# Kernel optimization log

Measured on AMD Instinct MI355X. Metric: run time of the kernel, lower is better.

## Reference

```python
import jax, jax.numpy as jnp
import numpy as np

B, S, HID = 4, 128, 4096
D, HQ, HK = 128, 32, 8
PAGES, PSIZE, NPP = 64, 256, 16  # page pool, page size, pages per sequence
THETA = 10000.0
EPS = 1e-6
SCALE = 1.0 / float(np.sqrt(D))


def setup_inputs() -> dict:
    key = jax.random.key(0)
    ks = jax.random.split(key, 10)
    x = jax.random.normal(ks[0], (B, S, HID), jnp.float32)
    Wq = jax.random.normal(ks[1], (HQ * D, HID), jnp.float32) * 0.02
    Wk = jax.random.normal(ks[2], (HK * D, HID), jnp.float32) * 0.02
    Wv = jax.random.normal(ks[3], (HK * D, HID), jnp.float32) * 0.02
    Wo = jax.random.normal(ks[4], (HID, HQ * D), jnp.float32) * 0.02
    q_norm_w = jax.random.uniform(ks[5], (D,), jnp.float32)
    k_norm_w = jax.random.uniform(ks[6], (D,), jnp.float32)
    k_cache = jax.random.normal(ks[7], (PAGES, PSIZE, HK, D), jnp.float32)
    v_cache = jax.random.normal(ks[8], (PAGES, PSIZE, HK, D), jnp.float32)
    block_table = jnp.arange(B * NPP, dtype=jnp.int32).reshape(B, NPP)
    cache_seqlens = jax.random.randint(ks[9], (B,), 0, 3800).astype(jnp.int32)
    return dict(x=x, Wq=Wq, Wk=Wk, Wv=Wv, Wo=Wo, q_norm_w=q_norm_w,
                k_norm_w=k_norm_w, k_cache=k_cache, v_cache=v_cache,
                block_table=block_table, cache_seqlens=cache_seqlens)


def _rmsnorm(t, w):
    # per-head RMSNorm over head_dim (constant_bias = 0)
    var = jnp.mean(t * t, axis=-1, keepdims=True)
    return t * jax.lax.rsqrt(var + EPS) * w


def _rope(t, pos):
    # NeoX-style half-rotation. t: [B,S,H,D], pos: [B,S]
    inv_freq = 1.0 / (THETA ** (jnp.arange(0, D, 2, dtype=jnp.float32) / D))  # [D/2]
    freqs = pos[..., None].astype(jnp.float32) * inv_freq                     # [B,S,D/2]
    cos = jnp.cos(freqs)[:, :, None, :]
    sin = jnp.sin(freqs)[:, :, None, :]
    t1, t2 = t[..., : D // 2], t[..., D // 2:]
    return jnp.concatenate([t1 * cos - t2 * sin, t2 * cos + t1 * sin], axis=-1)


def reference(x, Wq, Wk, Wv, Wo, q_norm_w, k_norm_w, k_cache, v_cache,
              block_table, cache_seqlens):
    bsz, seqlen, _ = x.shape
    # QKV projections
    q = jnp.einsum('bsd,ed->bse', x, Wq).reshape(bsz, seqlen, HQ, D)
    k = jnp.einsum('bsd,ed->bse', x, Wk).reshape(bsz, seqlen, HK, D)
    v = jnp.einsum('bsd,ed->bse', x, Wv).reshape(bsz, seqlen, HK, D)
    # QK-norm then RoPE (fused norm+rope path of the module)
    q = _rmsnorm(q, q_norm_w)
    k = _rmsnorm(k, k_norm_w)
    pos = cache_seqlens[:, None] + jnp.arange(seqlen)[None, :]  # [B,S]
    q = _rope(q, pos)
    k = _rope(k, pos)
    # Gather paged KV cache: [B, NPP*PSIZE, HK, D]
    L = NPP * PSIZE
    kc = k_cache[block_table].reshape(bsz, L, HK, D)
    vc = v_cache[block_table].reshape(bsz, L, HK, D)
    # Append new tokens (flash_attn_with_kvcache writes k,v into the cache)
    k_all = jnp.concatenate([kc, k], axis=1)  # [B, L+S, HK, D]
    v_all = jnp.concatenate([vc, v], axis=1)
    # Valid mask: cache slots < cache_seqlens; all new keys valid (causal=False, full window)
    valid_c = jnp.arange(L)[None, :] < cache_seqlens[:, None]          # [B, L]
    valid = jnp.concatenate(
        [valid_c, jnp.ones((bsz, seqlen), dtype=bool)], axis=1)        # [B, L+S]
    rep = HQ // HK
    k_all = jnp.repeat(k_all, rep, axis=2)
    v_all = jnp.repeat(v_all, rep, axis=2)
    scores = jnp.einsum('bqhd,bkhd->bhqk', q, k_all) * SCALE
    scores = jnp.where(valid[:, None, None, :], scores, -1e30)
    probs = jax.nn.softmax(scores, axis=-1)
    o = jnp.einsum('bhqk,bkhd->bqhd', probs, v_all)
    o = o.reshape(bsz, seqlen, HQ * D)
    return jnp.einsum('bse,de->bsd', o, Wo)
```

## Files before the change

### kernel.cpp

```cpp
#include <hip/hip_runtime.h>

typedef unsigned short u16;
typedef float f4v __attribute__((ext_vector_type(4)));
typedef short s8v __attribute__((ext_vector_type(8)));
typedef int   i4v __attribute__((ext_vector_type(4)));

#define SCALE_ 0.08838834764831845f
#define LOG2E_ 1.44269504088896340f

__device__ __forceinline__ u16 f2b(float f) {
    union { float f; unsigned u; } c; c.f = f;
    unsigned u = c.u + 0x7fffu + ((c.u >> 16) & 1u);
    return (u16)(u >> 16);
}

typedef const __attribute__((address_space(1))) unsigned int gu32;
typedef __attribute__((address_space(3))) unsigned int lu32;
__device__ __forceinline__ void glds16(const void* g, void* l) {
    __builtin_amdgcn_global_load_lds((gu32*)g, (lu32*)l, 16, 0, 0);
}

__device__ __forceinline__ int rho(int kv) {
    return (kv & 0x20) | ((kv & 0x04) << 2) | ((kv & 0x18) >> 1) | (kv & 3);
}

template <int RB>
__global__ __launch_bounds__(256) void wcvt_k(const float* __restrict__ src,
                                              u16* __restrict__ dst, int K) {
    const int kt = blockIdx.x, nt = blockIdx.y;
    u16* out = dst + ((size_t)nt * gridDim.x + kt) * (RB * 64);
#pragma unroll
    for (int i = 0; i < RB / 32; i++) {
        int c = threadIdx.x + i * 256;
        int r = c >> 3, c16 = c & 7, cc = c16 ^ (r & 7);
        const float* p = src + (size_t)(nt * RB + r) * K + kt * 64 + cc * 8;
        float4 f0 = *(const float4*)p, f1 = *(const float4*)(p + 4);
        s8v v;
        v[0] = (short)f2b(f0.x); v[1] = (short)f2b(f0.y);
        v[2] = (short)f2b(f0.z); v[3] = (short)f2b(f0.w);
        v[4] = (short)f2b(f1.x); v[5] = (short)f2b(f1.y);
        v[6] = (short)f2b(f1.z); v[7] = (short)f2b(f1.w);
        *(s8v*)(out + r * 64 + c16 * 8) = v;
    }
}

__global__ __launch_bounds__(256) void fgemm2(const u16* __restrict__ Ag,
                                              const u16* __restrict__ Bg,
                                              float* __restrict__ Cp,
                                              int M, int N, int K, int Ksl,
                                              int NY, int NZ) {
    __shared__ __align__(16) u16 As[2][4096];
    __shared__ __align__(16) u16 Bs[2][8192];
    const int tid = threadIdx.x, lane = tid & 63, wid = tid >> 6;
    const int lm = lane & 15, lg = lane >> 4;
    const int nb = gridDim.x, per = nb >> 3, w = blockIdx.x;
    const int idx = (w & 7) * per + (w >> 3);
    const int nx = idx / (NY * NZ);
    const int rem = idx - nx * (NY * NZ);
    const int my = rem % NY, z = rem / NY;
    const int m0 = my * 64, n0 = nx * 128;
    const int KT = K >> 6, NT = Ksl >> 6;
    const int kt0 = (z * Ksl) >> 6;
    const u16* ga = Ag + ((size_t)my * KT + kt0) * 4096;
    const u16* gb = Bg + ((size_t)nx * KT + kt0) * 8192;
    Cp += (size_t)z * M * N;

    f4v acc[4][2];
#pragma unroll
    for (int mi = 0; mi < 4; mi++)
#pragma unroll
        for (int ni = 0; ni < 2; ni++) acc[mi][ni] = (f4v){0.f, 0.f, 0.f, 0.f};

    auto STAGE = [&](int buf, int kt) {
        const char* a = (const char*)(ga + (size_t)kt * 4096) + tid * 16;
        const char* b = (const char*)(gb + (size_t)kt * 8192) + tid * 16;
        char* la = (char*)As[buf] + tid * 16;
        char* lb = (char*)Bs[buf] + tid * 16;
        glds16(a, la);
        glds16(a + 4096, la + 4096);
#pragma unroll
        for (int i = 0; i < 4; i++) glds16(b + i * 4096, lb + i * 4096);
    };

    STAGE(0, 0);
    asm volatile("s_waitcnt vmcnt(0)" ::: "memory");
    __syncthreads();

    for (int kt = 0; kt < NT; ++kt) {
        const int cur = kt & 1;
        if (kt + 1 < NT) STAGE(cur ^ 1, kt + 1);
#pragma unroll
        for (int ks = 0; ks < 2; ks++) {
            s8v av[4], bv[2];
#pragma unroll
            for (int mi = 0; mi < 4; mi++) {
                int r = mi * 16 + lm;
                av[mi] = *(const s8v*)(As[cur] + r * 64 + (((ks * 4 + lg) ^ (r & 7)) * 8));
            }
#pragma unroll
            for (int ni = 0; ni < 2; ni++) {
                int r = wid * 32 + ni * 16 + lm;
                bv[ni] = *(const s8v*)(Bs[cur] + r * 64 + (((ks * 4 + lg) ^ (r & 7)) * 8));
            }
#pragma unroll
            for (int mi = 0; mi < 4; mi++)
#pragma unroll
                for (int ni = 0; ni < 2; ni++)
                    acc[mi][ni] = __builtin_amdgcn_mfma_f32_16x16x32_bf16(av[mi], bv[ni], acc[mi][ni], 0, 0, 0);
        }
        asm volatile("s_waitcnt vmcnt(0)" ::: "memory");
        __syncthreads();
    }

#pragma unroll
    for (int mi = 0; mi < 4; mi++)
#pragma unroll
        for (int ni = 0; ni < 2; ni++)
#pragma unroll
            for (int r = 0; r < 4; r++) {
                int m = m0 + mi * 16 + lg * 4 + r;
                int n = n0 + wid * 32 + ni * 16 + lm;
                Cp[(size_t)m * N + n] = acc[mi][ni][r];
            }
}

__global__ __launch_bounds__(256) void nrope_k(const float* __restrict__ src,
                                               u16* __restrict__ dst,
                                               const float* __restrict__ w,
                                               const int* __restrict__ cseq,
                                               int nheads, float oscale,
                                               int nsl, size_t sls) {
    const int lane = threadIdx.x & 63;
    const int rid = blockIdx.x * 4 + (threadIdx.x >> 6);
    const int s = (rid / nheads) & 127;
    const int b = rid / (nheads * 128);
    const float* p = src + (size_t)rid * 128;
    float x1 = 0.f, x2 = 0.f;
    for (int sl = 0; sl < nsl; sl++) {
        x1 += p[sl * sls + lane];
        x2 += p[sl * sls + lane + 64];
    }
    float ss = x1 * x1 + x2 * x2;
#pragma unroll
    for (int off = 1; off < 64; off <<= 1) ss += __shfl_xor(ss, off);
    float inv = rsqrtf(ss * (1.0f / 128.0f) + 1e-6f);
    float n1 = x1 * inv * w[lane];
    float n2 = x2 * inv * w[lane + 64];
    float pos = (float)(cseq[b] + s);
    float ang = pos * powf(10000.0f, -(float)lane * (1.0f / 64.0f));
    float cs = cosf(ang), sn = sinf(ang);
    dst[(size_t)rid * 128 + lane]      = f2b((n1 * cs - n2 * sn) * oscale);
    dst[(size_t)rid * 128 + lane + 64] = f2b((n2 * cs + n1 * sn) * oscale);
}

__global__ __launch_bounds__(256) void cvt_bf16k(const float* __restrict__ s,
                                                 u16* __restrict__ d, int n4,
                                                 int nsl, size_t sls) {
    int i = blockIdx.x * blockDim.x + threadIdx.x;
    if (i < n4) {
        f4v f = (f4v){0.f, 0.f, 0.f, 0.f};
        for (int sl = 0; sl < nsl; sl++)
            f += *(const f4v*)(s + sl * sls + (size_t)i * 4);
        ushort4 o;
        o.x = f2b(f[0]); o.y = f2b(f[1]); o.z = f2b(f[2]); o.w = f2b(f[3]);
        ((ushort4*)d)[i] = o;
    }
}

__global__ __launch_bounds__(256) void red4_k(const float* __restrict__ p,
                                              float* __restrict__ out, int n4,
                                              size_t sls) {
    int i = blockIdx.x * blockDim.x + threadIdx.x;
    if (i < n4) {
        f4v s = (f4v){0.f, 0.f, 0.f, 0.f};
#pragma unroll
        for (int sl = 0; sl < 4; sl++)
            s += *(const f4v*)(p + sl * sls + (size_t)i * 4);
        *(f4v*)(out + (size_t)i * 4) = s;
    }
}

__global__ __launch_bounds__(256) void cvtkv_k(const float* __restrict__ kc,
                                               const float* __restrict__ vc,
                                               const u16* __restrict__ kb,
                                               const u16* __restrict__ vb,
                                               const int* __restrict__ btab,
                                               const int* __restrict__ cseq,
                                               u16* __restrict__ kb2,
                                               u16* __restrict__ vb2) {
    const int t = blockIdx.x, hk = blockIdx.y, b = blockIdx.z;
    const int tid = threadIdx.x;
    const int cl = cseq[b];
    if (t < 64 && t * 64 >= cl) return;
    u16* kout = kb2 + ((size_t)(b * 8 + hk) * 66 + t) * 8192;
    u16* vout = vb2 + ((size_t)(b * 8 + hk) * 66 + t) * 8192;

    if (t < 64) {
#pragma unroll
        for (int i = 0; i < 4; i++) {
            int c = tid + i * 256; int r = c >> 4, c16 = c & 15;
            int rs = rho(r);
            int cc = c16 ^ (rs & 7);
            int p = t * 64 + r;
            const float* src = kc + (((size_t)btab[b * 16 + (p >> 8)] * 256 + (p & 255)) * 8 + hk) * 128 + cc * 8;
            float4 f0 = *(const float4*)src, f1 = *(const float4*)(src + 4);
            s8v v;
            v[0] = (short)f2b(f0.x); v[1] = (short)f2b(f0.y); v[2] = (short)f2b(f0.z); v[3] = (short)f2b(f0.w);
            v[4] = (short)f2b(f1.x); v[5] = (short)f2b(f1.y); v[6] = (short)f2b(f1.z); v[7] = (short)f2b(f1.w);
            *(s8v*)(kout + rs * 128 + c16 * 8) = v;
        }
#pragma unroll
        for (int i = 0; i < 4; i++) {
            int c = tid + i * 256; int pr = c >> 5, c16v = c & 31;
            int nc = c16v ^ pr;
            int n = nc * 4;
            int p = t * 64 + pr * 2;
            const float* s0 = vc + (((size_t)btab[b * 16 + (p >> 8)] * 256 + (p & 255)) * 8 + hk) * 128 + n;
            float4 e = *(const float4*)s0, o = *(const float4*)(s0 + 1024);
            i4v w;
            w[0] = (int)((unsigned)f2b(e.x) | ((unsigned)f2b(o.x) << 16));
            w[1] = (int)((unsigned)f2b(e.y) | ((unsigned)f2b(o.y) << 16));
            w[2] = (int)((unsigned)f2b(e.z) | ((unsigned)f2b(o.z) << 16));
            w[3] = (int)((unsigned)f2b(e.w) | ((unsigned)f2b(o.w) << 16));
            *(i4v*)(vout + pr * 256 + c16v * 8) = w;
        }
    } else {
        int s0r = (t - 64) * 64;
#pragma unroll
        for (int i = 0; i < 4; i++) {
            int c = tid + i * 256; int r = c >> 4, c16 = c & 15;
            int rs = rho(r);
            int cc = c16 ^ (rs & 7);
            s8v v = *(const s8v*)(kb + ((size_t)(b * 128 + s0r + r) * 8 + hk) * 128 + cc * 8);
            *(s8v*)(kout + rs * 128 + c16 * 8) = v;
        }
#pragma unroll
        for (int i = 0; i < 4; i++) {
            int c = tid + i * 256; int pr = c >> 5, c16v = c & 31;
            int nc = c16v ^ pr;
            int n = nc * 4;
            const u16* s0 = vb + ((size_t)(b * 128 + s0r + pr * 2) * 8 + hk) * 128 + n;
            ushort4 e = *(const ushort4*)s0, o = *(const ushort4*)(s0 + 1024);
            i4v w;
            w[0] = (int)((unsigned)e.x | ((unsigned)o.x << 16));
            w[1] = (int)((unsigned)e.y | ((unsigned)o.y << 16));
            w[2] = (int)((unsigned)e.z | ((unsigned)o.z << 16));
            w[3] = (int)((unsigned)e.w | ((unsigned)o.w << 16));
            *(i4v*)(vout + pr * 256 + c16v * 8) = w;
        }
    }
}

__global__ __launch_bounds__(256) void fattn3_k(const u16* __restrict__ qb,
                                                const u16* __restrict__ kb2,
                                                const u16* __restrict__ vb2,
                                                const int* __restrict__ cseq,
                                                float* __restrict__ po,
                                                float* __restrict__ mb,
                                                float* __restrict__ lb) {
    __shared__ __align__(16) char Ks[2][16384];
    __shared__ __align__(16) char Vs[2][16384];

    const int tid = threadIdx.x, lane = tid & 63, wid = tid >> 6;
    const int lm = lane & 15, lg = lane >> 4;
    const int bid = blockIdx.x;
    const int sp = bid & 3, half = (bid >> 2) & 1, h = (bid >> 3) & 31, b = bid >> 8;
    const int hk = h >> 2;

    s8v qa[4];
    {
        const u16* qp = qb + ((size_t)((b * 128 + half * 64 + wid * 16 + lm) * 32 + h)) * 128 + lg * 8;
#pragma unroll
        for (int ks = 0; ks < 4; ks++) qa[ks] = *(const s8v*)(qp + ks * 32);
    }

    float m_run = -1e30f, l_run = 0.f;
    f4v acc[8];
#pragma unroll
    for (int dt = 0; dt < 8; dt++) acc[dt] = (f4v){0.f, 0.f, 0.f, 0.f};

    const int cl = cseq[b];
    const int ntc = (cl + 63) >> 6;
    const int tlo = (ntc * sp) >> 2, thi = (ntc * (sp + 1)) >> 2;
    const int ncache = thi - tlo;
    const int ntiles = ncache + (sp == 3 ? 2 : 0);

    const char* gk = (const char*)kb2 + (size_t)(b * 8 + hk) * 66 * 16384;
    const char* gv = (const char*)vb2 + (size_t)(b * 8 + hk) * 66 * 16384;

    auto STAGE = [&](int buf, int gt) {
        const char* gkt = gk + (size_t)gt * 16384 + wid * 4096 + lane * 16;
        const char* gvt = gv + (size_t)gt * 16384 + wid * 4096 + lane * 16;
        char* lk = Ks[buf] + wid * 4096;
        char* lv = Vs[buf] + wid * 4096;
#pragma unroll
        for (int i = 0; i < 4; i++) {
            glds16(gkt + i * 1024, lk + i * 1024);
            glds16(gvt + i * 1024, lv + i * 1024);
        }
    };
    auto GT = [&](int ii) { return ii < ncache ? tlo + ii : 64 + (ii - ncache); };

    if (ntiles > 0) STAGE(0, GT(0));
    asm volatile("s_waitcnt vmcnt(0)" ::: "memory");
    __syncthreads();

    for (int ii = 0; ii < ntiles; ++ii) {
        const int cur = ii & 1;
        if (ii + 1 < ntiles) STAGE(cur ^ 1, GT(ii + 1));
        const int gt = GT(ii);
        const int t0 = gt * 64;

        f4v sc[4];
#pragma unroll
        for (int ct = 0; ct < 4; ct++) sc[ct] = (f4v){0.f, 0.f, 0.f, 0.f};
        __builtin_amdgcn_s_setprio(1);
#pragma unroll
        for (int ct = 0; ct < 4; ct++) {
#pragma unroll
            for (int ks = 0; ks < 4; ks++) {
                int r = ct * 16 + lm;
                s8v kf = *(const s8v*)(Ks[cur] + ((r * 256 + ks * 64 + lg * 16) ^ ((r & 7) << 4)));
                sc[ct] = __builtin_amdgcn_mfma_f32_16x16x32_bf16(kf, qa[ks], sc[ct], 0, 0, 0);
            }
        }
        __builtin_amdgcn_s_setprio(0);

        if (gt < 64 && (t0 + 64 > cl)) {
#pragma unroll
            for (int ct = 0; ct < 4; ct++)
#pragma unroll
                for (int r = 0; r < 4; r++) {
                    int kvloc = (ct >> 1) * 32 + lg * 8 + (ct & 1) * 4 + r;
                    if (t0 + kvloc >= cl) sc[ct][r] = -1e30f;
                }
        }

        float mt = sc[0][0];
#pragma unroll
        for (int ct = 0; ct < 4; ct++)
#pragma unroll
            for (int r = 0; r < 4; r++) mt = fmaxf(mt, sc[ct][r]);
        mt = fmaxf(mt, __shfl_xor(mt, 16));
        mt = fmaxf(mt, __shfl_xor(mt, 32));

        if (__any(mt > m_run + 12.0f)) {
            float mn = fmaxf(m_run, mt);
            float corr = exp2f(m_run - mn);
            m_run = mn;
            l_run *= corr;
            float c0 = __shfl(corr, lg * 4 + 0);
            float c1 = __shfl(corr, lg * 4 + 1);
            float c2 = __shfl(corr, lg * 4 + 2);
            float c3 = __shfl(corr, lg * 4 + 3);
#pragma unroll
            for (int dt = 0; dt < 8; dt++) {
                acc[dt][0] *= c0; acc[dt][1] *= c1;
                acc[dt][2] *= c2; acc[dt][3] *= c3;
            }
        }

        short pb[4][4];
        float ladd = 0.f;
#pragma unroll
        for (int ct = 0; ct < 4; ct++)
#pragma unroll
            for (int r = 0; r < 4; r++) {
                float pv = exp2f(sc[ct][r] - m_run);
                ladd += pv;
                pb[ct][r] = (short)f2b(pv);
            }
        l_run += ladd;

        __builtin_amdgcn_s_setprio(1);
#pragma unroll
        for (int k2 = 0; k2 < 2; k2++) {
            s8v pa;
#pragma unroll
            for (int j = 0; j < 4; j++) { pa[j] = pb[2 * k2][j]; pa[4 + j] = pb[2 * k2 + 1][j]; }
#pragma unroll
            for (int dt = 0; dt < 8; dt++) {
                i4v vv;
#pragma unroll
                for (int t = 0; t < 4; t++) {
                    int p = k2 * 16 + lg * 4 + t;
                    vv[t] = *(const int*)(Vs[cur] + p * 512 + ((((dt * 16 + lm) * 4)) ^ ((p & 31) << 4)));
                }
                union { i4v i; s8v s; } u; u.i = vv;
                acc[dt] = __builtin_amdgcn_mfma_f32_16x16x32_bf16(pa, u.s, acc[dt], 0, 0, 0);
            }
        }
        __builtin_amdgcn_s_setprio(0);

        asm volatile("s_waitcnt vmcnt(0)" ::: "memory");
        __syncthreads();
    }

#pragma unroll
    for (int dt = 0; dt < 8; dt++) {
#pragma unroll
        for (int r = 0; r < 4; r++) {
            int row = wid * 16 + lg * 4 + r;
            po[((size_t)bid * 64 + row) * 128 + dt * 16 + lm] = acc[dt][r];
        }
    }
    float lt = l_run;
    lt += __shfl_xor(lt, 16);
    lt += __shfl_xor(lt, 32);
    if (lg == 0) {
        mb[(size_t)bid * 64 + wid * 16 + lm] = m_run;
        lb[(size_t)bid * 64 + wid * 16 + lm] = lt;
    }
}

__global__ __launch_bounds__(256) void fcomb_k(const float* __restrict__ po,
                                               const float* __restrict__ mb,
                                               const float* __restrict__ lb,
                                               u16* __restrict__ obT) {
    const int pid = blockIdx.x, t = threadIdx.x;
    const int row = t >> 2, dq = t & 3;
    const int half = pid & 1, h = (pid >> 1) & 31, b = pid >> 6;
    float m[4], l[4];
#pragma unroll
    for (int i = 0; i < 4; i++) {
        m[i] = mb[(size_t)(pid * 4 + i) * 64 + row];
        l[i] = lb[(size_t)(pid * 4 + i) * 64 + row];
    }
    float M = fmaxf(fmaxf(m[0], m[1]), fmaxf(m[2], m[3]));
    float w[4], L = 0.f;
#pragma unroll
    for (int i = 0; i < 4; i++) { w[i] = exp2f(m[i] - M); L += w[i] * l[i]; }
    float invL = 1.0f / L;
    const int arow = b * 128 + half * 64 + row;
    const int mt = arow >> 6, rr = arow & 63;
#pragma unroll
    for (int j = 0; j < 8; j++) {
        f4v s = (f4v){0.f, 0.f, 0.f, 0.f};
#pragma unroll
        for (int i = 0; i < 4; i++) {
            f4v a = *(const f4v*)(po + ((size_t)(pid * 4 + i) * 64 + row) * 128 + dq * 32 + j * 4);
            s += w[i] * a;
        }
        ushort4 o;
        o.x = f2b(s[0] * invL); o.y = f2b(s[1] * invL);
        o.z = f2b(s[2] * invL); o.w = f2b(s[3] * invL);
        const int acol = h * 128 + dq * 32 + j * 4;
        const int kt = acol >> 6, cch = (acol >> 3) & 7, wo = acol & 7;
        *(ushort4*)(obT + ((size_t)(mt * 64 + kt)) * 4096 + rr * 64 + ((cch ^ (rr & 7)) * 8) + wo) = o;
    }
}

extern "C" void kernel_launch(void* const* d_in, const int* in_sizes, int n_in,
                              void* d_out, int out_size, void* d_ws, size_t ws_size,
                              hipStream_t stream) {
    const float* x   = (const float*)d_in[0];
    const float* Wq  = (const float*)d_in[1];
    const float* Wk  = (const float*)d_in[2];
    const float* Wv  = (const float*)d_in[3];
    const float* Wo  = (const float*)d_in[4];
    const float* qnw = (const float*)d_in[5];
    const float* knw = (const float*)d_in[6];
    const float* kc  = (const float*)d_in[7];
    const float* vc  = (const float*)d_in[8];
    const int* btab  = (const int*)d_in[9];
    const int* cseq  = (const int*)d_in[10];
    float* out = (float*)d_out;

    char* ws = (char*)d_ws;
    u16*   qb   = (u16*)(ws + 0);
    u16*   kb   = (u16*)(ws + 4194304);
    u16*   vb   = (u16*)(ws + 5242880);
    u16*   obT  = (u16*)(ws + 6291456);
    u16*   xb   = (u16*)(ws + 6291456);
    float* mbuf = (float*)(ws + 10485760);
    float* lbuf = (float*)(ws + 10747904);
    float* P    = (float*)(ws + 11010048);
    u16*   wW   = (u16*)(ws + 44564480);
    u16*   kb2  = (u16*)(ws + 44564480);
    u16*   vb2  = (u16*)(ws + 79167488);

    dim3 blk(256, 1, 1);
    const size_t slsQ = (size_t)512 * 4096, slsKV = (size_t)512 * 1024;

    wcvt_k<64><<<dim3(64, 8, 1), blk, 0, stream>>>(x, xb, 4096);

    wcvt_k<128><<<dim3(64, 32, 1), blk, 0, stream>>>(Wq, wW, 4096);
    fgemm2<<<dim3(1024, 1, 1), blk, 0, stream>>>(xb, wW, P, 512, 4096, 4096, 1024, 8, 4);
    nrope_k<<<dim3(4096, 1, 1), blk, 0, stream>>>(P, qb, qnw, cseq, 32, SCALE_ * LOG2E_, 4, slsQ);

    wcvt_k<128><<<dim3(64, 8, 1), blk, 0, stream>>>(Wk, wW, 4096);
    fgemm2<<<dim3(512, 1, 1), blk, 0, stream>>>(xb, wW, P, 512, 1024, 4096, 512, 8, 8);
    nrope_k<<<dim3(1024, 1, 1), blk, 0, stream>>>(P, kb, knw, cseq, 8, 1.0f, 8, slsKV);

    wcvt_k<128><<<dim3(64, 8, 1), blk, 0, stream>>>(Wv, wW, 4096);
    fgemm2<<<dim3(512, 1, 1), blk, 0, stream>>>(xb, wW, P, 512, 1024, 4096, 512, 8, 8);
    cvt_bf16k<<<dim3(512, 1, 1), blk, 0, stream>>>(P, vb, 131072, 8, slsKV);

    cvtkv_k<<<dim3(66, 8, 4), blk, 0, stream>>>(kc, vc, kb, vb, btab, cseq, kb2, vb2);
    fattn3_k<<<dim3(1024, 1, 1), blk, 0, stream>>>(qb, kb2, vb2, cseq, P, mbuf, lbuf);
    fcomb_k<<<dim3(256, 1, 1), blk, 0, stream>>>(P, mbuf, lbuf, obT);

    wcvt_k<128><<<dim3(64, 32, 1), blk, 0, stream>>>(Wo, wW, 4096);
    fgemm2<<<dim3(1024, 1, 1), blk, 0, stream>>>(obT, wW, P, 512, 4096, 4096, 1024, 8, 4);
    red4_k<<<dim3(2048, 1, 1), blk, 0, stream>>>(P, out, 2097152, slsQ);
}
```

Before: 262.1 us.

## Process both query halves per attention block to reuse staged KV tiles

The attention kernel now handles both 64-row query halves for a given batch, head and split in one block, so each KV tile staged into LDS serves 128 query rows instead of 64. The grid halves from 1024 to 512 blocks, and partial outputs are written to the same virtual block slots so the combine kernel is unchanged. This halves global KV traffic and staging work, but doubles per-thread accumulator and Q registers, which may lower occupancy, and leaves fewer blocks to spread across the CUs.

After: 288.9 us. 10.2% more time.

```diff
diff --git a/kernel.cpp b/kernel.cpp
--- a/kernel.cpp
+++ b/kernel.cpp
@@ -251,7 +251,7 @@
     }
 }
 
-__global__ __launch_bounds__(256) void fattn3_k(const u16* __restrict__ qb,
+__global__ __launch_bounds__(256) void fattn5_k(const u16* __restrict__ qb,
                                                 const u16* __restrict__ kb2,
                                                 const u16* __restrict__ vb2,
                                                 const int* __restrict__ cseq,
@@ -264,20 +264,23 @@
     const int tid = threadIdx.x, lane = tid & 63, wid = tid >> 6;
     const int lm = lane & 15, lg = lane >> 4;
     const int bid = blockIdx.x;
-    const int sp = bid & 3, half = (bid >> 2) & 1, h = (bid >> 3) & 31, b = bid >> 8;
+    const int sp = bid & 3, h = (bid >> 2) & 31, b = bid >> 7;
     const int hk = h >> 2;
 
-    s8v qa[4];
-    {
-        const u16* qp = qb + ((size_t)((b * 128 + half * 64 + wid * 16 + lm) * 32 + h)) * 128 + lg * 8;
-#pragma unroll
-        for (int ks = 0; ks < 4; ks++) qa[ks] = *(const s8v*)(qp + ks * 32);
-    }
-
-    float m_run = -1e30f, l_run = 0.f;
-    f4v acc[8];
-#pragma unroll
-    for (int dt = 0; dt < 8; dt++) acc[dt] = (f4v){0.f, 0.f, 0.f, 0.f};
+    s8v qa[2][4];
+#pragma unroll
+    for (int hf = 0; hf < 2; hf++) {
+        const u16* qp = qb + ((size_t)((b * 128 + hf * 64 + wid * 16 + lm) * 32 + h)) * 128 + lg * 8;
+#pragma unroll
+        for (int ks = 0; ks < 4; ks++) qa[hf][ks] = *(const s8v*)(qp + ks * 32);
+    }
+
+    float m_run[2] = {-1e30f, -1e30f}, l_run[2] = {0.f, 0.f};
+    f4v acc[2][8];
+#pragma unroll
+    for (int hf = 0; hf < 2; hf++)
+#pragma unroll
+        for (int dt = 0; dt < 8; dt++) acc[hf][dt] = (f4v){0.f, 0.f, 0.f, 0.f};
 
     const int cl = cseq[b];
     const int ntc = (cl + 63) >> 6;
@@ -311,105 +314,112 @@
         const int gt = GT(ii);
         const int t0 = gt * 64;
 
-        f4v sc[4];
-#pragma unroll
-        for (int ct = 0; ct < 4; ct++) sc[ct] = (f4v){0.f, 0.f, 0.f, 0.f};
-        __builtin_amdgcn_s_setprio(1);
-#pragma unroll
-        for (int ct = 0; ct < 4; ct++) {
-#pragma unroll
-            for (int ks = 0; ks < 4; ks++) {
-                int r = ct * 16 + lm;
-                s8v kf = *(const s8v*)(Ks[cur] + ((r * 256 + ks * 64 + lg * 16) ^ ((r & 7) << 4)));
-                sc[ct] = __builtin_amdgcn_mfma_f32_16x16x32_bf16(kf, qa[ks], sc[ct], 0, 0, 0);
-            }
-        }
-        __builtin_amdgcn_s_setprio(0);
-
-        if (gt < 64 && (t0 + 64 > cl)) {
+#pragma unroll
+        for (int hf = 0; hf < 2; hf++) {
+            f4v sc[4];
+#pragma unroll
+            for (int ct = 0; ct < 4; ct++) sc[ct] = (f4v){0.f, 0.f, 0.f, 0.f};
+            __builtin_amdgcn_s_setprio(1);
+#pragma unroll
+            for (int ct = 0; ct < 4; ct++) {
+#pragma unroll
+                for (int ks = 0; ks < 4; ks++) {
+                    int r = ct * 16 + lm;
+                    s8v kf = *(const s8v*)(Ks[cur] + ((r * 256 + ks * 64 + lg * 16) ^ ((r & 7) << 4)));
+                    sc[ct] = __builtin_amdgcn_mfma_f32_16x16x32_bf16(kf, qa[hf][ks], sc[ct], 0, 0, 0);
+                }
+            }
+            __builtin_amdgcn_s_setprio(0);
+
+            if (gt < 64 && (t0 + 64 > cl)) {
+#pragma unroll
+                for (int ct = 0; ct < 4; ct++)
+#pragma unroll
+                    for (int r = 0; r < 4; r++) {
+                        int kvloc = (ct >> 1) * 32 + lg * 8 + (ct & 1) * 4 + r;
+                        if (t0 + kvloc >= cl) sc[ct][r] = -1e30f;
+                    }
+            }
+
+            float mt = sc[0][0];
 #pragma unroll
             for (int ct = 0; ct < 4; ct++)
 #pragma unroll
+                for (int r = 0; r < 4; r++) mt = fmaxf(mt, sc[ct][r]);
+            mt = fmaxf(mt, __shfl_xor(mt, 16));
+            mt = fmaxf(mt, __shfl_xor(mt, 32));
+
+            if (__any(mt > m_run[hf] + 12.0f)) {
+                float mn = fmaxf(m_run[hf], mt);
+                float corr = exp2f(m_run[hf] - mn);
+                m_run[hf] = mn;
+                l_run[hf] *= corr;
+                float c0 = __shfl(corr, lg * 4 + 0);
+                float c1 = __shfl(corr, lg * 4 + 1);
+                float c2 = __shfl(corr, lg * 4 + 2);
+                float c3 = __shfl(corr, lg * 4 + 3);
+#pragma unroll
+                for (int dt = 0; dt < 8; dt++) {
+                    acc[hf][dt][0] *= c0; acc[hf][dt][1] *= c1;
+                    acc[hf][dt][2] *= c2; acc[hf][dt][3] *= c3;
+                }
+            }
+
+            short pb[4][4];
+            float ladd = 0.f;
+#pragma unroll
+            for (int ct = 0; ct < 4; ct++)
+#pragma unroll
                 for (int r = 0; r < 4; r++) {
-                    int kvloc = (ct >> 1) * 32 + lg * 8 + (ct & 1) * 4 + r;
-                    if (t0 + kvloc >= cl) sc[ct][r] = -1e30f;
+                    float pv = exp2f(sc[ct][r] - m_run[hf]);
+                    ladd += pv;
+                    pb[ct][r] = (short)f2b(pv);
                 }
-        }
-
-        float mt = sc[0][0];
-#pragma unroll
-        for (int ct = 0; ct < 4; ct++)
-#pragma unroll
-            for (int r = 0; r < 4; r++) mt = fmaxf(mt, sc[ct][r]);
-        mt = fmaxf(mt, __shfl_xor(mt, 16));
-        mt = fmaxf(mt, __shfl_xor(mt, 32));
-
-        if (__any(mt > m_run + 12.0f)) {
-            float mn = fmaxf(m_run, mt);
-            float corr = exp2f(m_run - mn);
-            m_run = mn;
-            l_run *= corr;
-            float c0 = __shfl(corr, lg * 4 + 0);
-            float c1 = __shfl(corr, lg * 4 + 1);
-            float c2 = __shfl(corr, lg * 4 + 2);
-            float c3 = __shfl(corr, lg * 4 + 3);
-#pragma unroll
-            for (int dt = 0; dt < 8; dt++) {
-                acc[dt][0] *= c0; acc[dt][1] *= c1;
-                acc[dt][2] *= c2; acc[dt][3] *= c3;
-            }
-        }
-
-        short pb[4][4];
-        float ladd = 0.f;
-#pragma unroll
-        for (int ct = 0; ct < 4; ct++)
-#pragma unroll
-            for (int r = 0; r < 4; r++) {
-                float pv = exp2f(sc[ct][r] - m_run);
-                ladd += pv;
-                pb[ct][r] = (short)f2b(pv);
-            }
-        l_run += ladd;
-
-        __builtin_amdgcn_s_setprio(1);
-#pragma unroll
-        for (int k2 = 0; k2 < 2; k2++) {
-            s8v pa;
-#pragma unroll
-            for (int j = 0; j < 4; j++) { pa[j] = pb[2 * k2][j]; pa[4 + j] = pb[2 * k2 + 1][j]; }
-#pragma unroll
-            for (int dt = 0; dt < 8; dt++) {
-                i4v vv;
-#pragma unroll
-                for (int t = 0; t < 4; t++) {
-                    int p = k2 * 16 + lg * 4 + t;
-                    vv[t] = *(const int*)(Vs[cur] + p * 512 + ((((dt * 16 + lm) * 4)) ^ ((p & 31) << 4)));
+            l_run[hf] += ladd;
+
+            __builtin_amdgcn_s_setprio(1);
+#pragma unroll
+            for (int k2 = 0; k2 < 2; k2++) {
+                s8v pa;
+#pragma unroll
+                for (int j = 0; j < 4; j++) { pa[j] = pb[2 * k2][j]; pa[4 + j] = pb[2 * k2 + 1][j]; }
+#pragma unroll
+                for (int dt = 0; dt < 8; dt++) {
+                    i4v vv;
+#pragma unroll
+                    for (int t = 0; t < 4; t++) {
+                        int p = k2 * 16 + lg * 4 + t;
+                        vv[t] = *(const int*)(Vs[cur] + p * 512 + ((((dt * 16 + lm) * 4)) ^ ((p & 31) << 4)));
+                    }
+                    union { i4v i; s8v s; } u; u.i = vv;
+                    acc[hf][dt] = __builtin_amdgcn_mfma_f32_16x16x32_bf16(pa, u.s, acc[hf][dt], 0, 0, 0);
                 }
-                union { i4v i; s8v s; } u; u.i = vv;
-                acc[dt] = __builtin_amdgcn_mfma_f32_16x16x32_bf16(pa, u.s, acc[dt], 0, 0, 0);
-            }
-        }
-        __builtin_amdgcn_s_setprio(0);
+            }
+            __builtin_amdgcn_s_setprio(0);
+        }
 
         asm volatile("s_waitcnt vmcnt(0)" ::: "memory");
         __syncthreads();
     }
 
 #pragma unroll
-    for (int dt = 0; dt < 8; dt++) {
-#pragma unroll
-        for (int r = 0; r < 4; r++) {
-            int row = wid * 16 + lg * 4 + r;
-            po[((size_t)bid * 64 + row) * 128 + dt * 16 + lm] = acc[dt][r];
-        }
-    }
-    float lt = l_run;
-    lt += __shfl_xor(lt, 16);
-    lt += __shfl_xor(lt, 32);
-    if (lg == 0) {
-        mb[(size_t)bid * 64 + wid * 16 + lm] = m_run;
-        lb[(size_t)bid * 64 + wid * 16 + lm] = lt;
+    for (int hf = 0; hf < 2; hf++) {
+        const size_t vbid = (size_t)(b * 256 + h * 8 + hf * 4 + sp);
+#pragma unroll
+        for (int dt = 0; dt < 8; dt++) {
+#pragma unroll
+            for (int r = 0; r < 4; r++) {
+                int row = wid * 16 + lg * 4 + r;
+                po[(vbid * 64 + row) * 128 + dt * 16 + lm] = acc[hf][dt][r];
+            }
+        }
+        float lt = l_run[hf];
+        lt += __shfl_xor(lt, 16);
+        lt += __shfl_xor(lt, 32);
+        if (lg == 0) {
+            mb[vbid * 64 + wid * 16 + lm] = m_run[hf];
+            lb[vbid * 64 + wid * 16 + lm] = lt;
+        }
     }
 }
 
@@ -497,7 +507,7 @@
     cvt_bf16k<<<dim3(512, 1, 1), blk, 0, stream>>>(P, vb, 131072, 8, slsKV);
 
     cvtkv_k<<<dim3(66, 8, 4), blk, 0, stream>>>(kc, vc, kb, vb, btab, cseq, kb2, vb2);
-    fattn3_k<<<dim3(1024, 1, 1), blk, 0, stream>>>(qb, kb2, vb2, cseq, P, mbuf, lbuf);
+    fattn5_k<<<dim3(512, 1, 1), blk, 0, stream>>>(qb, kb2, vb2, cseq, P, mbuf, lbuf);
     fcomb_k<<<dim3(256, 1, 1), blk, 0, stream>>>(P, mbuf, lbuf, obT);
 
     wcvt_k<128><<<dim3(64, 32, 1), blk, 0, stream>>>(Wo, wW, 4096);
```
